# Kernel tuning notes

Hardware: AMD Instinct MI355X
Metric: run time of the kernel (lower is better)

Reference implementation:

```python
import jax, jax.numpy as jnp
import numpy as np

N, E, D, H, G, O = 50000, 800000, 128, 256, 128, 10
BN_EPS = 1e-5
SLOPE = 0.2  # LeakyReLU negative slope


def setup_inputs() -> dict:
    keys = iter(jax.random.split(jax.random.key(0), 64))

    def rn(shape, scale=0.05):
        return jax.random.normal(next(keys), shape, jnp.float32) * scale

    inp = {
        "x": jax.random.normal(next(keys), (N, D), jnp.float32),
        "edge_index": jax.random.randint(next(keys), (2, E), 0, N),
        "edge_attr": jax.random.normal(next(keys), (E, 3), jnp.float32),
        "batch": jnp.sort(jax.random.randint(next(keys), (N,), 0, G)),
    }
    for i, din in zip((1, 2, 3), (D, H, H)):
        inp[f"We{i}"] = rn((3, din))
        inp[f"be{i}"] = jnp.zeros((din,), jnp.float32)
        inp[f"W{i}1"] = rn((din, H))
        inp[f"b{i}1"] = jnp.zeros((H,), jnp.float32)
        inp[f"g{i}"] = jnp.ones((H,), jnp.float32)
        inp[f"bt{i}"] = jnp.zeros((H,), jnp.float32)
        inp[f"mu{i}"] = jnp.zeros((H,), jnp.float32)
        inp[f"var{i}"] = jnp.ones((H,), jnp.float32)
        inp[f"W{i}2"] = rn((H, H))
        inp[f"b{i}2"] = jnp.zeros((H,), jnp.float32)
    for name, shape in (("Wm1", (3 * H, 200)), ("Wm2", (200, 200)), ("Wm3", (200, 200)), ("Wm4", (200, O))):
        inp[name] = rn(shape)
        inp["b" + name[1:]] = jnp.zeros((shape[1],), jnp.float32)
    return inp


def _leaky(v):
    return jax.nn.leaky_relu(v, SLOPE)


def _gine(x, src, dst, ea, We, be, W1, b1, g, bt, mu, var, W2, b2):
    # message: ReLU(x_j + lin_edge(edge_attr)); aggregate: scatter-sum to dst
    msg = jax.nn.relu(x[src] + ea @ We + be)          # [E, din]
    agg = jax.ops.segment_sum(msg, dst, num_segments=N)  # [N, din]
    h = x + agg                                       # (1+eps)*x_i + agg, eps=0
    h = h @ W1 + b1
    h = g * (h - mu) * jax.lax.rsqrt(var + BN_EPS) + bt  # BatchNorm1d (eval)
    h = _leaky(h)
    return _leaky(h @ W2 + b2)


def reference(x, edge_index, edge_attr, batch,
              We1, be1, W11, b11, g1, bt1, mu1, var1, W12, b12,
              We2, be2, W21, b21, g2, bt2, mu2, var2, W22, b22,
              We3, be3, W31, b31, g3, bt3, mu3, var3, W32, b32,
              Wm1, bm1, Wm2, bm2, Wm3, bm3, Wm4, bm4):
    src, dst = edge_index[0], edge_index[1]
    x1 = _gine(x, src, dst, edge_attr, We1, be1, W11, b11, g1, bt1, mu1, var1, W12, b12)
    x2 = _gine(x1, src, dst, edge_attr, We2, be2, W21, b21, g2, bt2, mu2, var2, W22, b22)
    x3 = _gine(x2, src, dst, edge_attr, We3, be3, W31, b31, g3, bt3, mu3, var3, W32, b32)
    p1 = jax.ops.segment_sum(x1, batch, num_segments=G)  # global_add_pool
    p2 = jax.ops.segment_sum(x2, batch, num_segments=G)
    p3 = jax.ops.segment_sum(x3, batch, num_segments=G)
    h = jnp.concatenate((p1, p2, p3), axis=1)            # [G, 3H]
    # MLP (dropout is identity at inference); note doubled LeakyReLU in source
    h = _leaky(_leaky(h @ Wm1 + bm1))
    h = _leaky(_leaky(h @ Wm2 + bm2))
    h = _leaky(_leaky(h @ Wm3 + bm3))
    return h @ Wm4 + bm4                                 # [G, O]
```

## Files before the change

kernel.cpp:

```cpp
#include <hip/hip_runtime.h>
#include <hip/hip_fp16.h>

#define LRELU(v) ((v) >= 0.f ? (v) : 0.2f * (v))
#define DLRELU(v) ((v) >= 0.f ? (v) : 0.04f * (v))

constexpr int Nn = 50000;
constexpr int Ee = 800000;
constexpr int Hh = 256;
constexpr int Gg = 128;
constexpr int Oo = 10;

typedef __attribute__((ext_vector_type(8))) short short8;
typedef __attribute__((ext_vector_type(4))) float f32x4;
typedef __attribute__((ext_vector_type(4))) unsigned int uv4;
typedef __attribute__((ext_vector_type(2))) unsigned int uv2;
typedef __attribute__((ext_vector_type(4))) unsigned short us4;

__device__ inline unsigned short f2h(float f) {
  __half h = __float2half_rn(f);
  return *reinterpret_cast<unsigned short*>(&h);
}
__device__ inline float h2f(unsigned short u) {
  __half h = *reinterpret_cast<__half*>(&u);
  return __half2float(h);
}
__device__ inline __half2 u2h2(unsigned int u) {
  return *reinterpret_cast<__half2*>(&u);
}
__device__ inline unsigned int h22u(__half2 h) {
  return *reinterpret_cast<unsigned int*>(&h);
}
__device__ inline __half2 hmax2(__half2 a, __half2 b) {
  __half2 r;
  asm volatile("v_pk_max_f16 %0, %1, %2" : "=v"(r) : "v"(a), "v"(b));
  return r;
}
__device__ inline unsigned short f2bf(float f) {
  union { float f; unsigned int i; } v; v.f = f;
  unsigned int i = v.i;
  return (unsigned short)((i + 0x7FFFu + ((i >> 16) & 1u)) >> 16);
}

typedef __attribute__((address_space(1))) const unsigned int gu32;
typedef __attribute__((address_space(3))) unsigned int lu32;
__device__ inline void gload_lds16(const void* g, void* l) {
  __builtin_amdgcn_global_load_lds((gu32*)g, (lu32*)l, 16, 0, 0);
}

__global__ __launch_bounds__(256) void hist_kernel(
    const int* __restrict__ dst, int* __restrict__ deg)
{
  const int e = blockIdx.x * 256 + threadIdx.x;
  if (e < Ee) atomicAdd(&deg[dst[e]], 1);
}

__global__ __launch_bounds__(1024) void scan1_kernel(
    const int* __restrict__ deg, int* __restrict__ bsum)
{
  const int i = blockIdx.x * 1024 + threadIdx.x;
  int v = (i < Nn) ? deg[i] : 0;
  #pragma unroll
  for (int o = 32; o; o >>= 1) v += __shfl_xor(v, o, 64);
  __shared__ int ws[16];
  const int wid = threadIdx.x >> 6, lane = threadIdx.x & 63;
  if (lane == 0) ws[wid] = v;
  __syncthreads();
  if (threadIdx.x == 0) {
    int s = 0;
    #pragma unroll
    for (int k = 0; k < 16; k++) s += ws[k];
    bsum[blockIdx.x] = s;
  }
}

__global__ __launch_bounds__(64) void scan2_kernel(
    const int* __restrict__ bsum, int* __restrict__ boff, int* __restrict__ row_ptr, int nb)
{
  if (threadIdx.x == 0) {
    int s = 0;
    for (int b = 0; b < nb; b++) { boff[b] = s; s += bsum[b]; }
    row_ptr[Nn] = s;
  }
}

__global__ __launch_bounds__(1024) void scan3_kernel(
    const int* __restrict__ deg, const int* __restrict__ boff,
    int* __restrict__ row_ptr, int* __restrict__ cursor)
{
  const int i = blockIdx.x * 1024 + threadIdx.x;
  const int wid = threadIdx.x >> 6, lane = threadIdx.x & 63;
  const int v = (i < Nn) ? deg[i] : 0;
  int inc = v;
  #pragma unroll
  for (int o = 1; o < 64; o <<= 1) {
    const int u = __shfl_up(inc, o, 64);
    if (lane >= o) inc += u;
  }
  __shared__ int ws[16];
  if (lane == 63) ws[wid] = inc;
  __syncthreads();
  if (wid == 0 && lane < 16) {
    int s = ws[lane];
    #pragma unroll
    for (int o = 1; o < 16; o <<= 1) {
      const int u = __shfl_up(s, o, 64);
      if (lane >= o) s += u;
    }
    ws[lane] = s;
  }
  __syncthreads();
  const int woff = (wid == 0) ? 0 : ws[wid - 1];
  const int excl = boff[blockIdx.x] + woff + inc - v;
  if (i < Nn) { row_ptr[i] = excl; cursor[i] = excl; }
}

__global__ __launch_bounds__(256) void fill_kernel(
    const int* __restrict__ src, const int* __restrict__ dst,
    const float* __restrict__ ea, int* __restrict__ cursor,
    uv4* __restrict__ edges)
{
  const int e = blockIdx.x * 256 + threadIdx.x;
  if (e >= Ee) return;
  const int pos = atomicAdd(&cursor[dst[e]], 1);
  uv4 r;
  r.x = (unsigned)src[e];
  r.y = h22u(__float2half2_rn(ea[3 * e + 0]));
  r.z = h22u(__float2half2_rn(ea[3 * e + 1]));
  r.w = h22u(__float2half2_rn(ea[3 * e + 2]));
  edges[pos] = r;
}

__global__ __launch_bounds__(256) void f2h_kernel(
    const float* __restrict__ in, unsigned short* __restrict__ out, int n4)
{
  const int i = blockIdx.x * 256 + threadIdx.x;
  if (i >= n4) return;
  const float4 v = *reinterpret_cast<const float4*>(in + (size_t)i * 4);
  us4 o; o.x = f2h(v.x); o.y = f2h(v.y); o.z = f2h(v.z); o.w = f2h(v.w);
  *reinterpret_cast<us4*>(out + (size_t)i * 4) = o;
}

__global__ __launch_bounds__(256) void f2bf_kernel(
    const float* __restrict__ in, unsigned short* __restrict__ out, int n4)
{
  const int i = blockIdx.x * 256 + threadIdx.x;
  if (i >= n4) return;
  const float4 v = *reinterpret_cast<const float4*>(in + (size_t)i * 4);
  us4 o; o.x = f2bf(v.x); o.y = f2bf(v.y); o.z = f2bf(v.z); o.w = f2bf(v.w);
  *reinterpret_cast<us4*>(out + (size_t)i * 4) = o;
}

struct WtJobs {
  const float* src[10];
  unsigned short* dst[10];
  int K[10], M[10], Kpad[10], isbf[10], blk0[11];
};

__global__ __launch_bounds__(256) void wtall_kernel(WtJobs J)
{
  int j = 0;
  #pragma unroll
  for (int q = 1; q < 10; q++) if ((int)blockIdx.x >= J.blk0[q]) j = q;
  const int g = ((int)blockIdx.x - J.blk0[j]) * 256 + threadIdx.x;
  const int Kpad = J.Kpad[j];
  if (g >= 256 * Kpad) return;
  const int c = g / Kpad, k = g % Kpad;
  const int K = J.K[j], M = J.M[j];
  unsigned short o = 0;
  if (c < M && k < K) {
    const float w = J.src[j][(size_t)k * M + c];
    o = J.isbf[j] ? f2bf(w) : f2h(w);
  }
  J.dst[j][(size_t)c * Kpad + k] = o;
}

template<int DIN>
__global__ __launch_bounds__(256) void agg_gather(
    const unsigned short* __restrict__ x, const uv4* __restrict__ edges,
    const float* __restrict__ We, const float* __restrict__ be,
    const int* __restrict__ row_ptr, unsigned short* __restrict__ S)
{
  constexpr int FPL = DIN / 64;
  constexpr int H2  = FPL / 2;
  constexpr int SH  = (DIN == 256) ? 8 : 7;
  const int wv   = threadIdx.x >> 6;
  const int lane = threadIdx.x & 63;
  const int n = blockIdx.x * 4 + wv;
  if (n >= Nn) return;
  const int fo = lane * FPL;

  const __half2 zero2 = __float2half2_rn(0.f);
  __half2 w0h[H2], w1h[H2], w2h[H2], bbh[H2], acc[H2];
  #pragma unroll
  for (int j = 0; j < H2; j++) {
    w0h[j] = __halves2half2(__float2half_rn(We[0 * DIN + fo + 2 * j]),
                            __float2half_rn(We[0 * DIN + fo + 2 * j + 1]));
    w1h[j] = __halves2half2(__float2half_rn(We[1 * DIN + fo + 2 * j]),
                            __float2half_rn(We[1 * DIN + fo + 2 * j + 1]));
    w2h[j] = __halves2half2(__float2half_rn(We[2 * DIN + fo + 2 * j]),
                            __float2half_rn(We[2 * DIN + fo + 2 * j + 1]));
    bbh[j] = __halves2half2(__float2half_rn(be[fo + 2 * j]),
                            __float2half_rn(be[fo + 2 * j + 1]));
    acc[j] = zero2;
  }

  const int beg = row_ptr[n], end = row_ptr[n + 1];
  int i = beg;

  for (; i + 4 <= end; i += 4) {
    uv4 e[4];
    #pragma unroll
    for (int q = 0; q < 4; q++) e[q] = __builtin_nontemporal_load(edges + i + q);
    __half2 xv[4][H2];
    #pragma unroll
    for (int q = 0; q < 4; q++) {
      const unsigned o = (e[q].x << SH) + fo;
      if constexpr (H2 == 2) {
        const uv2 r = *reinterpret_cast<const uv2*>(x + o);
        xv[q][0] = u2h2(r.x); xv[q][1] = u2h2(r.y);
      } else {
        xv[q][0] = u2h2(*reinterpret_cast<const unsigned int*>(x + o));
      }
    }
    #pragma unroll
    for (int q = 0; q < 4; q++) {
      const __half2 a0 = u2h2(e[q].y), a1 = u2h2(e[q].z), a2 = u2h2(e[q].w);
      #pragma unroll
      for (int j = 0; j < H2; j++) {
        __half2 m = __hadd2(xv[q][j], bbh[j]);
        m = __hfma2(a2, w2h[j], m);
        m = __hfma2(a1, w1h[j], m);
        m = __hfma2(a0, w0h[j], m);
        acc[j] = __hadd2(acc[j], hmax2(m, zero2));
      }
    }
  }
  for (; i < end; i++) {
    const uv4 e0 = __builtin_nontemporal_load(edges + i);
    const unsigned o0 = (e0.x << SH) + fo;
    __half2 xv0[H2];
    if constexpr (H2 == 2) {
      const uv2 r0 = *reinterpret_cast<const uv2*>(x + o0);
      xv0[0] = u2h2(r0.x); xv0[1] = u2h2(r0.y);
    } else {
      xv0[0] = u2h2(*reinterpret_cast<const unsigned int*>(x + o0));
    }
    const __half2 a00 = u2h2(e0.y), a01 = u2h2(e0.z), a02 = u2h2(e0.w);
    #pragma unroll
    for (int j = 0; j < H2; j++) {
      __half2 m0 = __hadd2(xv0[j], bbh[j]);
      m0 = __hfma2(a02, w2h[j], m0);
      m0 = __hfma2(a01, w1h[j], m0);
      m0 = __hfma2(a00, w0h[j], m0);
      acc[j] = __hadd2(acc[j], hmax2(m0, zero2));
    }
  }

  const unsigned on = ((unsigned)n << SH) + fo;
  if constexpr (H2 == 2) {
    const uv2 rs = *reinterpret_cast<const uv2*>(x + on);
    const float2 s0 = __half22float2(u2h2(rs.x)), s1 = __half22float2(u2h2(rs.y));
    const float2 f0 = __half22float2(acc[0]), f1 = __half22float2(acc[1]);
    uv2 o;
    o.x = (unsigned)f2h(s0.x + f0.x) | ((unsigned)f2h(s0.y + f0.y) << 16);
    o.y = (unsigned)f2h(s1.x + f1.x) | ((unsigned)f2h(s1.y + f1.y) << 16);
    __builtin_nontemporal_store(o, reinterpret_cast<uv2*>(S + on));
  } else {
    const float2 s0 = __half22float2(u2h2(*reinterpret_cast<const unsigned int*>(x + on)));
    const float2 f0 = __half22float2(acc[0]);
    const unsigned o = (unsigned)f2h(s0.x + f0.x) | ((unsigned)f2h(s0.y + f0.y) << 16);
    __builtin_nontemporal_store(o, reinterpret_cast<unsigned int*>(S + on));
  }
}

template<int K, bool DOBN>
__global__ __launch_bounds__(512) void gemm_mfma(
    const unsigned short* __restrict__ A, const unsigned short* __restrict__ Bt,
    const float* __restrict__ bias,
    const float* __restrict__ gamma, const float* __restrict__ beta,
    const float* __restrict__ mu, const float* __restrict__ var,
    unsigned short* __restrict__ C)
{
  __shared__ __align__(16) unsigned short lA[128 * 64];
  __shared__ __align__(16) unsigned short lB[256 * 64];
  const int t = threadIdx.x;
  const int lane = t & 63, wid = t >> 6;
  const int wrow = wid >> 2, wcol = wid & 3;
  const int l15 = lane & 15, hi = lane >> 4;
  const int n0 = blockIdx.y * 128;
  const int srow = lane >> 3;
  const int sslot = lane & 7;

  f32x4 acc[4][4] = {};

  for (int k0 = 0; k0 < K; k0 += 64) {
    #pragma unroll
    for (int c = 0; c < 6; c++) {
      const int chunk = wid * 6 + c;
      if (chunk < 16) {
        const int row = chunk * 8 + srow;
        const int scol = (sslot ^ (row & 7)) * 8;
        const int gr = min(n0 + row, Nn - 1);
        gload_lds16(A + (size_t)gr * K + k0 + scol, (char*)lA + chunk * 1024);
      } else {
        const int bchunk = chunk - 16;
        const int row = bchunk * 8 + srow;
        const int scol = (sslot ^ (row & 7)) * 8;
        gload_lds16(Bt + (size_t)row * K + k0 + scol, (char*)lB + bchunk * 1024);
      }
    }
    __syncthreads();
    #pragma unroll
    for (int kk = 0; kk < 2; kk++) {
      short8 av[4], bv[4];
      #pragma unroll
      for (int rf = 0; rf < 4; rf++) {
        const int ar = wrow * 64 + rf * 16 + l15;
        av[rf] = *reinterpret_cast<const short8*>(
            (const char*)lA + ar * 128 + (((kk * 4 + hi) ^ (ar & 7)) << 4));
      }
      #pragma unroll
      for (int cf = 0; cf < 4; cf++) {
        const int br = wcol * 64 + cf * 16 + l15;
        bv[cf] = *reinterpret_cast<const short8*>(
            (const char*)lB + br * 128 + (((kk * 4 + hi) ^ (br & 7)) << 4));
      }
      #pragma unroll
      for (int rf = 0; rf < 4; rf++)
        #pragma unroll
        for (int cf = 0; cf < 4; cf++)
          acc[rf][cf] = __builtin_amdgcn_mfma_f32_16x16x32_f16(av[rf], bv[cf], acc[rf][cf], 0, 0, 0);
    }
    __syncthreads();
  }

  #pragma unroll
  for (int cf = 0; cf < 4; cf++) {
    const int col = wcol * 64 + cf * 16 + l15;
    const float bs = bias[col];
    float gm = 0.f, bt2 = 0.f, mm = 0.f, iv = 0.f;
    if constexpr (DOBN) {
      gm = gamma[col]; bt2 = beta[col]; mm = mu[col];
      iv = rsqrtf(var[col] + 1e-5f);
    }
    #pragma unroll
    for (int rf = 0; rf < 4; rf++) {
      #pragma unroll
      for (int rg = 0; rg < 4; rg++) {
        const int row = n0 + wrow * 64 + rf * 16 + hi * 4 + rg;
        if (row >= Nn) continue;
        float v = acc[rf][cf][rg] + bs;
        if constexpr (DOBN) v = gm * (v - mm) * iv + bt2;
        v = LRELU(v);
        C[(size_t)row * 256 + col] = f2h(v);
      }
    }
  }
}

__global__ __launch_bounds__(256) void pool_kernel(
    const unsigned short* __restrict__ xl, const int* __restrict__ batch,
    float* __restrict__ pooled, int layer)
{
  constexpr int NPB = 16;
  const int n0 = blockIdx.x * NPB;
  const int c  = threadIdx.x;
  if (n0 >= Nn) return;
  float acc = 0.f;
  int curb = batch[n0];
  for (int i = 0; i < NPB; i++) {
    const int n = n0 + i;
    if (n >= Nn) break;
    const int b = batch[n];
    if (b != curb) {
      atomicAdd(pooled + (size_t)curb * 768 + layer * 256 + c, acc);
      acc = 0.f;
      curb = b;
    }
    acc += h2f(xl[(size_t)n * 256 + c]);
  }
  atomicAdd(pooled + (size_t)curb * 768 + layer * 256 + c, acc);
}

__global__ __launch_bounds__(256) void head_fused(
    const unsigned short* __restrict__ P,
    const unsigned short* __restrict__ B1t,
    const unsigned short* __restrict__ B2t,
    const unsigned short* __restrict__ B3t,
    const unsigned short* __restrict__ B4t,
    const float* __restrict__ b1, const float* __restrict__ b2,
    const float* __restrict__ b3, const float* __restrict__ b4,
    float* __restrict__ out)
{
  __shared__ __align__(16) unsigned short act[32 * 256];
  const int t = threadIdx.x, lane = t & 63, wid = t >> 6;
  const int l15 = lane & 15, hi = lane >> 4;
  const int r0 = blockIdx.x * 32;

  f32x4 acc[2][4];

  #pragma unroll
  for (int rf = 0; rf < 2; rf++)
    #pragma unroll
    for (int cf = 0; cf < 4; cf++) acc[rf][cf] = (f32x4){0.f, 0.f, 0.f, 0.f};
  #pragma unroll 2
  for (int ks = 0; ks < 24; ks++) {
    short8 bv[4], av[2];
    #pragma unroll
    for (int cf = 0; cf < 4; cf++) {
      const int c = wid * 64 + cf * 16 + l15;
      bv[cf] = *reinterpret_cast<const short8*>(B1t + (size_t)c * 768 + ks * 32 + hi * 8);
    }
    #pragma unroll
    for (int rf = 0; rf < 2; rf++)
      av[rf] = *reinterpret_cast<const short8*>(
          P + (size_t)(r0 + rf * 16 + l15) * 768 + ks * 32 + hi * 8);
    #pragma unroll
    for (int rf = 0; rf < 2; rf++)
      #pragma unroll
      for (int cf = 0; cf < 4; cf++)
        acc[rf][cf] = __builtin_amdgcn_mfma_f32_16x16x32_bf16(av[rf], bv[cf], acc[rf][cf], 0, 0, 0);
  }
  #pragma unroll
  for (int cf = 0; cf < 4; cf++) {
    const int c = wid * 64 + cf * 16 + l15;
    const float bs = (c < 200) ? b1[c] : 0.f;
    const int slot0 = c >> 3;
    #pragma unroll
    for (int rf = 0; rf < 2; rf++)
      #pragma unroll
      for (int rg = 0; rg < 4; rg++) {
        const int row = rf * 16 + hi * 4 + rg;
        const float v = DLRELU(acc[rf][cf][rg] + bs);
        act[row * 256 + ((slot0 ^ (row & 7)) << 3) + (c & 7)] = f2bf(v);
      }
  }
  __syncthreads();

  #pragma unroll
  for (int L = 0; L < 2; L++) {
    const unsigned short* B = (L == 0) ? B2t : B3t;
    const float* bias = (L == 0) ? b2 : b3;
    #pragma unroll
    for (int rf = 0; rf < 2; rf++)
      #pragma unroll
      for (int cf = 0; cf < 4; cf++) acc[rf][cf] = (f32x4){0.f, 0.f, 0.f, 0.f};
    #pragma unroll
    for (int ks = 0; ks < 8; ks++) {
      short8 bv[4], av[2];
      #pragma unroll
      for (int cf = 0; cf < 4; cf++) {
        const int c = wid * 64 + cf * 16 + l15;
        bv[cf] = *reinterpret_cast<const short8*>(B + (size_t)c * 256 + ks * 32 + hi * 8);
      }
      #pragma unroll
      for (int rf = 0; rf < 2; rf++) {
        const int row = rf * 16 + l15;
        const int slot = ks * 4 + hi;
        av[rf] = *reinterpret_cast<const short8*>(
            act + row * 256 + ((slot ^ (row & 7)) << 3));
      }
      #pragma unroll
      for (int rf = 0; rf < 2; rf++)
        #pragma unroll
        for (int cf = 0; cf < 4; cf++)
          acc[rf][cf] = __builtin_amdgcn_mfma_f32_16x16x32_bf16(av[rf], bv[cf], acc[rf][cf], 0, 0, 0);
    }
    __syncthreads();
    #pragma unroll
    for (int cf = 0; cf < 4; cf++) {
      const int c = wid * 64 + cf * 16 + l15;
      const float bs = (c < 200) ? bias[c] : 0.f;
      const int slot0 = c >> 3;
      #pragma unroll
      for (int rf = 0; rf < 2; rf++)
        #pragma unroll
        for (int rg = 0; rg < 4; rg++) {
          const int row = rf * 16 + hi * 4 + rg;
          const float v = DLRELU(acc[rf][cf][rg] + bs);
          act[row * 256 + ((slot0 ^ (row & 7)) << 3) + (c & 7)] = f2bf(v);
        }
    }
    __syncthreads();
  }

  if (wid == 0) {
    f32x4 a4[2] = {};
    #pragma unroll
    for (int ks = 0; ks < 8; ks++) {
      short8 av[2];
      const short8 bv = *reinterpret_cast<const short8*>(
          B4t + (size_t)l15 * 256 + ks * 32 + hi * 8);
      #pragma unroll
      for (int rf = 0; rf < 2; rf++) {
        const int row = rf * 16 + l15;
        const int slot = ks * 4 + hi;
        av[rf] = *reinterpret_cast<const short8*>(
            act + row * 256 + ((slot ^ (row & 7)) << 3));
      }
      #pragma unroll
      for (int rf = 0; rf < 2; rf++)
        a4[rf] = __builtin_amdgcn_mfma_f32_16x16x32_bf16(av[rf], bv, a4[rf], 0, 0, 0);
    }
    if (l15 < Oo) {
      const float bs = b4[l15];
      #pragma unroll
      for (int rf = 0; rf < 2; rf++)
        #pragma unroll
        for (int rg = 0; rg < 4; rg++) {
          const int row = r0 + rf * 16 + hi * 4 + rg;
          out[(size_t)row * Oo + l15] = a4[rf][rg] + bs;
        }
    }
  }
}

extern "C" void kernel_launch(void* const* d_in, const int* in_sizes, int n_in,
                              void* d_out, int out_size, void* d_ws, size_t ws_size,
                              hipStream_t stream)
{
  const float* x     = (const float*)d_in[0];
  const int*   ei    = (const int*)d_in[1];
  const float* ea    = (const float*)d_in[2];
  const int*   batch = (const int*)d_in[3];
  const int* src = ei;
  const int* dst = ei + Ee;

  const float *We[3], *be_[3], *W1[3], *b1[3], *g_[3], *bt_[3], *mu_[3], *var_[3], *W2[3], *b2[3];
  for (int l = 0; l < 3; l++) {
    const int base = 4 + l * 10;
    We[l]  = (const float*)d_in[base + 0];
    be_[l] = (const float*)d_in[base + 1];
    W1[l]  = (const float*)d_in[base + 2];
    b1[l]  = (const float*)d_in[base + 3];
    g_[l]  = (const float*)d_in[base + 4];
    bt_[l] = (const float*)d_in[base + 5];
    mu_[l] = (const float*)d_in[base + 6];
    var_[l]= (const float*)d_in[base + 7];
    W2[l]  = (const float*)d_in[base + 8];
    b2[l]  = (const float*)d_in[base + 9];
  }
  const float *Wm[4], *bm[4];
  for (int i = 0; i < 4; i++) {
    Wm[i] = (const float*)d_in[34 + 2 * i];
    bm[i] = (const float*)d_in[35 + 2 * i];
  }

  int* deg     = (int*)d_ws;
  int* cursor  = deg + Nn;
  int* row_ptr = cursor + Nn;
  int* bsum    = row_ptr + Nn + 4;
  int* boff    = bsum + 64;
  uv4* edges   = (uv4*)(boff + 64);
  unsigned short* x0h  = (unsigned short*)(edges + Ee);
  unsigned short* Wt11 = x0h + (size_t)Nn * 128;
  unsigned short* Wt12 = Wt11 + 32768;
  unsigned short* Wt21 = Wt12 + 65536;
  unsigned short* Wt22 = Wt21 + 65536;
  unsigned short* Wt31 = Wt22 + 65536;
  unsigned short* Wt32 = Wt31 + 65536;
  unsigned short* HW1t = Wt32 + 65536;
  unsigned short* HW2t = HW1t + 256 * 768;
  unsigned short* HW3t = HW2t + 65536;
  unsigned short* HW4t = HW3t + 65536;
  unsigned short* S    = HW4t + 65536;
  unsigned short* Y    = S  + (size_t)Nn * Hh;
  unsigned short* XB0  = Y  + (size_t)Nn * Hh;
  unsigned short* XB1  = XB0 + (size_t)Nn * Hh;
  unsigned short* Pbf  = XB1 + (size_t)Nn * Hh;
  float* pooled = (float*)(Pbf + (size_t)Gg * 768);
  float* outf  = (float*)d_out;

  const dim3 gemmGrid(1, (Nn + 127) / 128);
  const int  poolGrid = (Nn + 15) / 16;
  const int  aggGrid  = (Nn + 3) / 4;
  const int  eGrid    = (Ee + 255) / 256;
  const int  sGrid    = (Nn + 1023) / 1024;

  hipMemsetAsync(deg, 0, Nn * sizeof(int), stream);
  hipMemsetAsync(pooled, 0, (size_t)Gg * 768 * sizeof(float), stream);

  hist_kernel<<<eGrid, 256, 0, stream>>>(dst, deg);
  scan1_kernel<<<sGrid, 1024, 0, stream>>>(deg, bsum);
  scan2_kernel<<<1, 64, 0, stream>>>(bsum, boff, row_ptr, sGrid);
  scan3_kernel<<<sGrid, 1024, 0, stream>>>(deg, boff, row_ptr, cursor);
  fill_kernel<<<eGrid, 256, 0, stream>>>(src, dst, ea, cursor, edges);

  f2h_kernel<<<(Nn * 128 / 4 + 255) / 256, 256, 0, stream>>>(x, x0h, Nn * 128 / 4);
  {
    WtJobs J;
    const float* s[10] = {W1[0], W2[0], W1[1], W2[1], W1[2], W2[2], Wm[0], Wm[1], Wm[2], Wm[3]};
    unsigned short* d[10] = {Wt11, Wt12, Wt21, Wt22, Wt31, Wt32, HW1t, HW2t, HW3t, HW4t};
    const int Ks[10]   = {128, 256, 256, 256, 256, 256, 768, 200, 200, 200};
    const int Ms[10]   = {256, 256, 256, 256, 256, 256, 200, 200, 200, 10};
    const int Kp[10]   = {128, 256, 256, 256, 256, 256, 768, 256, 256, 256};
    const int bf[10]   = {0, 0, 0, 0, 0, 0, 1, 1, 1, 1};
    int blk = 0;
    for (int q = 0; q < 10; q++) {
      J.src[q] = s[q]; J.dst[q] = d[q];
      J.K[q] = Ks[q]; J.M[q] = Ms[q]; J.Kpad[q] = Kp[q]; J.isbf[q] = bf[q];
      J.blk0[q] = blk;
      blk += (256 * Kp[q] + 255) / 256;
    }
    J.blk0[10] = blk;
    wtall_kernel<<<blk, 256, 0, stream>>>(J);
  }

  agg_gather<128><<<aggGrid, 256, 0, stream>>>(x0h, edges, We[0], be_[0], row_ptr, S);
  gemm_mfma<128, true><<<gemmGrid, 512, 0, stream>>>(
      S, Wt11, b1[0], g_[0], bt_[0], mu_[0], var_[0], Y);
  gemm_mfma<256, false><<<gemmGrid, 512, 0, stream>>>(
      Y, Wt12, b2[0], nullptr, nullptr, nullptr, nullptr, XB0);
  pool_kernel<<<poolGrid, 256, 0, stream>>>(XB0, batch, pooled, 0);

  agg_gather<256><<<aggGrid, 256, 0, stream>>>(XB0, edges, We[1], be_[1], row_ptr, S);
  gemm_mfma<256, true><<<gemmGrid, 512, 0, stream>>>(
      S, Wt21, b1[1], g_[1], bt_[1], mu_[1], var_[1], Y);
  gemm_mfma<256, false><<<gemmGrid, 512, 0, stream>>>(
      Y, Wt22, b2[1], nullptr, nullptr, nullptr, nullptr, XB1);
  pool_kernel<<<poolGrid, 256, 0, stream>>>(XB1, batch, pooled, 1);

  agg_gather<256><<<aggGrid, 256, 0, stream>>>(XB1, edges, We[2], be_[2], row_ptr, S);
  gemm_mfma<256, true><<<gemmGrid, 512, 0, stream>>>(
      S, Wt31, b1[2], g_[2], bt_[2], mu_[2], var_[2], Y);
  gemm_mfma<256, false><<<gemmGrid, 512, 0, stream>>>(
      Y, Wt32, b2[2], nullptr, nullptr, nullptr, nullptr, XB0);
  pool_kernel<<<poolGrid, 256, 0, stream>>>(XB0, batch, pooled, 2);

  f2bf_kernel<<<(Gg * 768 / 4 + 255) / 256, 256, 0, stream>>>(pooled, Pbf, Gg * 768 / 4);
  head_fused<<<4, 256, 0, stream>>>(Pbf, HW1t, HW2t, HW3t, HW4t,
                                    bm[0], bm[1], bm[2], bm[3], outf);
}
```

Measured before the change: 621.4 us.

## Fuse the two per-layer MLP GEMMs into one kernel keeping intermediate in LDS

Merges the two GEMMs of each GINE layer's MLP into a single kernel. The whole 128-row A tile is loaded into LDS once, and the BN+LeakyReLU intermediate is written back to LDS (swizzled) and consumed by the second GEMM, so the Y round trip through global memory and one launch per layer disappear. B operands are now read directly from global or cache instead of being staged through LDS. The cost is 64KB of LDS per block, which lowers occupancy, and uncoalesced, cache-dependent weight loads.

```diff
diff --git a/kernel.cpp b/kernel.cpp
--- a/kernel.cpp
+++ b/kernel.cpp
@@ -273,88 +273,121 @@
   }
 }
 
-template<int K, bool DOBN>
-__global__ __launch_bounds__(512) void gemm_mfma(
-    const unsigned short* __restrict__ A, const unsigned short* __restrict__ Bt,
-    const float* __restrict__ bias,
+template<int K1>
+__global__ __launch_bounds__(512) void gemm12(
+    const unsigned short* __restrict__ A,
+    const unsigned short* __restrict__ B1t, const float* __restrict__ b1,
     const float* __restrict__ gamma, const float* __restrict__ beta,
     const float* __restrict__ mu, const float* __restrict__ var,
-    unsigned short* __restrict__ C)
-{
-  __shared__ __align__(16) unsigned short lA[128 * 64];
-  __shared__ __align__(16) unsigned short lB[256 * 64];
+    const unsigned short* __restrict__ B2t, const float* __restrict__ b2,
+    unsigned short* __restrict__ XB)
+{
+  __shared__ __align__(16) unsigned short smem[128 * 256];
+  unsigned short* lA = smem;
+  unsigned short* lY = smem;
+
   const int t = threadIdx.x;
   const int lane = t & 63, wid = t >> 6;
   const int wrow = wid >> 2, wcol = wid & 3;
   const int l15 = lane & 15, hi = lane >> 4;
-  const int n0 = blockIdx.y * 128;
-  const int srow = lane >> 3;
-  const int sslot = lane & 7;
+  const int n0 = blockIdx.x * 128;
+
+  constexpr int SPR = K1 / 8;
+  constexpr int NCH = 128 * K1 * 2 / 1024;
+  constexpr int CPW = NCH / 8;
+  #pragma unroll
+  for (int c = 0; c < CPW; c++) {
+    const int ch = wid * CPW + c;
+    const int row = ch * (512 / K1) + lane / SPR;
+    const int slot = lane % SPR;
+    const int scol = (slot ^ (row & 7)) * 8;
+    const int gr = min(n0 + row, Nn - 1);
+    gload_lds16(A + (size_t)gr * K1 + scol, (char*)lA + ch * 1024);
+  }
+  __syncthreads();
 
   f32x4 acc[4][4] = {};
-
-  for (int k0 = 0; k0 < K; k0 += 64) {
-    #pragma unroll
-    for (int c = 0; c < 6; c++) {
-      const int chunk = wid * 6 + c;
-      if (chunk < 16) {
-        const int row = chunk * 8 + srow;
-        const int scol = (sslot ^ (row & 7)) * 8;
-        const int gr = min(n0 + row, Nn - 1);
-        gload_lds16(A + (size_t)gr * K + k0 + scol, (char*)lA + chunk * 1024);
-      } else {
-        const int bchunk = chunk - 16;
-        const int row = bchunk * 8 + srow;
-        const int scol = (sslot ^ (row & 7)) * 8;
-        gload_lds16(Bt + (size_t)row * K + k0 + scol, (char*)lB + bchunk * 1024);
-      }
-    }
-    __syncthreads();
-    #pragma unroll
-    for (int kk = 0; kk < 2; kk++) {
-      short8 av[4], bv[4];
-      #pragma unroll
-      for (int rf = 0; rf < 4; rf++) {
-        const int ar = wrow * 64 + rf * 16 + l15;
-        av[rf] = *reinterpret_cast<const short8*>(
-            (const char*)lA + ar * 128 + (((kk * 4 + hi) ^ (ar & 7)) << 4));
-      }
-      #pragma unroll
-      for (int cf = 0; cf < 4; cf++) {
-        const int br = wcol * 64 + cf * 16 + l15;
-        bv[cf] = *reinterpret_cast<const short8*>(
-            (const char*)lB + br * 128 + (((kk * 4 + hi) ^ (br & 7)) << 4));
-      }
-      #pragma unroll
-      for (int rf = 0; rf < 4; rf++)
-        #pragma unroll
-        for (int cf = 0; cf < 4; cf++)
-          acc[rf][cf] = __builtin_amdgcn_mfma_f32_16x16x32_f16(av[rf], bv[cf], acc[rf][cf], 0, 0, 0);
-    }
-    __syncthreads();
+  #pragma unroll
+  for (int ks = 0; ks < K1 / 32; ks++) {
+    short8 av[4], bv[4];
+    #pragma unroll
+    for (int rf = 0; rf < 4; rf++) {
+      const int ar = wrow * 64 + rf * 16 + l15;
+      av[rf] = *reinterpret_cast<const short8*>(
+          (const char*)lA + ar * (K1 * 2) + (((ks * 4 + hi) ^ (ar & 7)) << 4));
+    }
+    #pragma unroll
+    for (int cf = 0; cf < 4; cf++) {
+      const int c = wcol * 64 + cf * 16 + l15;
+      bv[cf] = *reinterpret_cast<const short8*>(B1t + (size_t)c * K1 + ks * 32 + hi * 8);
+    }
+    #pragma unroll
+    for (int rf = 0; rf < 4; rf++)
+      #pragma unroll
+      for (int cf = 0; cf < 4; cf++)
+        acc[rf][cf] = __builtin_amdgcn_mfma_f32_16x16x32_f16(av[rf], bv[cf], acc[rf][cf], 0, 0, 0);
+  }
+  __syncthreads();
+
+  #pragma unroll
+  for (int cf = 0; cf < 4; cf++) {
+    const int c = wcol * 64 + cf * 16 + l15;
+    const float bs = b1[c];
+    const float gm = gamma[c], bt2 = beta[c], mm = mu[c];
+    const float iv = rsqrtf(var[c] + 1e-5f);
+    const int slot0 = c >> 3;
+    #pragma unroll
+    for (int rf = 0; rf < 4; rf++)
+      #pragma unroll
+      for (int rg = 0; rg < 4; rg++) {
+        const int row = wrow * 64 + rf * 16 + hi * 4 + rg;
+        float v = acc[rf][cf][rg] + bs;
+        v = gm * (v - mm) * iv + bt2;
+        v = LRELU(v);
+        *reinterpret_cast<unsigned short*>(
+            (char*)lY + row * 512 + (((slot0 ^ (row & 7)) << 4)) + (c & 7) * 2) = f2h(v);
+      }
+  }
+  __syncthreads();
+
+  #pragma unroll
+  for (int rf = 0; rf < 4; rf++)
+    #pragma unroll
+    for (int cf = 0; cf < 4; cf++) acc[rf][cf] = (f32x4){0.f, 0.f, 0.f, 0.f};
+  #pragma unroll
+  for (int ks = 0; ks < 8; ks++) {
+    short8 av[4], bv[4];
+    #pragma unroll
+    for (int rf = 0; rf < 4; rf++) {
+      const int ar = wrow * 64 + rf * 16 + l15;
+      av[rf] = *reinterpret_cast<const short8*>(
+          (const char*)lY + ar * 512 + (((ks * 4 + hi) ^ (ar & 7)) << 4));
+    }
+    #pragma unroll
+    for (int cf = 0; cf < 4; cf++) {
+      const int c = wcol * 64 + cf * 16 + l15;
+      bv[cf] = *reinterpret_cast<const short8*>(B2t + (size_t)c * 256 + ks * 32 + hi * 8);
+    }
+    #pragma unroll
+    for (int rf = 0; rf < 4; rf++)
+      #pragma unroll
+      for (int cf = 0; cf < 4; cf++)
+        acc[rf][cf] = __builtin_amdgcn_mfma_f32_16x16x32_f16(av[rf], bv[cf], acc[rf][cf], 0, 0, 0);
   }
 
   #pragma unroll
   for (int cf = 0; cf < 4; cf++) {
     const int col = wcol * 64 + cf * 16 + l15;
-    const float bs = bias[col];
-    float gm = 0.f, bt2 = 0.f, mm = 0.f, iv = 0.f;
-    if constexpr (DOBN) {
-      gm = gamma[col]; bt2 = beta[col]; mm = mu[col];
-      iv = rsqrtf(var[col] + 1e-5f);
-    }
-    #pragma unroll
-    for (int rf = 0; rf < 4; rf++) {
+    const float bs = b2[col];
+    #pragma unroll
+    for (int rf = 0; rf < 4; rf++)
       #pragma unroll
       for (int rg = 0; rg < 4; rg++) {
         const int row = n0 + wrow * 64 + rf * 16 + hi * 4 + rg;
         if (row >= Nn) continue;
-        float v = acc[rf][cf][rg] + bs;
-        if constexpr (DOBN) v = gm * (v - mm) * iv + bt2;
-        v = LRELU(v);
-        C[(size_t)row * 256 + col] = f2h(v);
-      }
-    }
+        const float v = LRELU(acc[rf][cf][rg] + bs);
+        XB[(size_t)row * 256 + col] = f2h(v);
+      }
   }
 }
 
@@ -564,14 +597,13 @@
   unsigned short* HW3t = HW2t + 65536;
   unsigned short* HW4t = HW3t + 65536;
   unsigned short* S    = HW4t + 65536;
-  unsigned short* Y    = S  + (size_t)Nn * Hh;
-  unsigned short* XB0  = Y  + (size_t)Nn * Hh;
+  unsigned short* XB0  = S  + (size_t)Nn * Hh;
   unsigned short* XB1  = XB0 + (size_t)Nn * Hh;
   unsigned short* Pbf  = XB1 + (size_t)Nn * Hh;
   float* pooled = (float*)(Pbf + (size_t)Gg * 768);
   float* outf  = (float*)d_out;
 
-  const dim3 gemmGrid(1, (Nn + 127) / 128);
+  const int  gemmGrid = (Nn + 127) / 128;
   const int  poolGrid = (Nn + 15) / 16;
   const int  aggGrid  = (Nn + 3) / 4;
   const int  eGrid    = (Ee + 255) / 256;
@@ -607,24 +639,18 @@
   }
 
   agg_gather<128><<<aggGrid, 256, 0, stream>>>(x0h, edges, We[0], be_[0], row_ptr, S);
-  gemm_mfma<128, true><<<gemmGrid, 512, 0, stream>>>(
-      S, Wt11, b1[0], g_[0], bt_[0], mu_[0], var_[0], Y);
-  gemm_mfma<256, false><<<gemmGrid, 512, 0, stream>>>(
-      Y, Wt12, b2[0], nullptr, nullptr, nullptr, nullptr, XB0);
+  gemm12<128><<<gemmGrid, 512, 0, stream>>>(
+      S, Wt11, b1[0], g_[0], bt_[0], mu_[0], var_[0], Wt12, b2[0], XB0);
   pool_kernel<<<poolGrid, 256, 0, stream>>>(XB0, batch, pooled, 0);
 
   agg_gather<256><<<aggGrid, 256, 0, stream>>>(XB0, edges, We[1], be_[1], row_ptr, S);
-  gemm_mfma<256, true><<<gemmGrid, 512, 0, stream>>>(
-      S, Wt21, b1[1], g_[1], bt_[1], mu_[1], var_[1], Y);
-  gemm_mfma<256, false><<<gemmGrid, 512, 0, stream>>>(
-      Y, Wt22, b2[1], nullptr, nullptr, nullptr, nullptr, XB1);
+  gemm12<256><<<gemmGrid, 512, 0, stream>>>(
+      S, Wt21, b1[1], g_[1], bt_[1], mu_[1], var_[1], Wt22, b2[1], XB1);
   pool_kernel<<<poolGrid, 256, 0, stream>>>(XB1, batch, pooled, 1);
 
   agg_gather<256><<<aggGrid, 256, 0, stream>>>(XB1, edges, We[2], be_[2], row_ptr, S);
-  gemm_mfma<256, true><<<gemmGrid, 512, 0, stream>>>(
-      S, Wt31, b1[2], g_[2], bt_[2], mu_[2], var_[2], Y);
-  gemm_mfma<256, false><<<gemmGrid, 512, 0, stream>>>(
-      Y, Wt32, b2[2], nullptr, nullptr, nullptr, nullptr, XB0);
+  gemm12<256><<<gemmGrid, 512, 0, stream>>>(
+      S, Wt31, b1[2], g_[2], bt_[2], mu_[2], var_[2], Wt32, b2[2], XB0);
   pool_kernel<<<poolGrid, 256, 0, stream>>>(XB0, batch, pooled, 2);
 
   f2bf_kernel<<<(Gg * 768 / 4 + 255) / 256, 256, 0, stream>>>(pooled, Pbf, Gg * 768 / 4);
```

Result: faster. 583.2 us (-6.1%).
